# Kernel optimization log

Measured on AMD Instinct MI355X. Metric: run time of the kernel, lower is better.

Reference implementation:

```python
import jax, jax.numpy as jnp
import numpy as np

NUM_DAYOFWEEK, NUM_TIME, NUM_MONTH, NUM_DAY = 7, 24, 12, 31
NUM_DESTINATION = 100000
NUM_FACTOR = 128
NUM_DIM = NUM_FACTOR // 4  # 32
N = 1048576


def setup_inputs() -> dict:
    key = jax.random.key(0)
    ks = jax.random.split(key, 10)
    std = 0.1
    return {
        "dayofweek": jax.random.randint(ks[0], (N,), 0, NUM_DAYOFWEEK),
        "time": jax.random.randint(ks[1], (N,), 0, NUM_TIME),
        "month": jax.random.randint(ks[2], (N,), 0, NUM_MONTH),
        "day": jax.random.randint(ks[3], (N,), 0, NUM_DAY),
        "destination": jax.random.randint(ks[4], (N,), 0, NUM_DESTINATION),
        "W_dayofweek": std * jax.random.normal(ks[5], (NUM_DAYOFWEEK, NUM_DIM), dtype=jnp.float32),
        "W_time": std * jax.random.normal(ks[6], (NUM_TIME, NUM_DIM), dtype=jnp.float32),
        "W_month": std * jax.random.normal(ks[7], (NUM_MONTH, NUM_DIM), dtype=jnp.float32),
        "W_day": std * jax.random.normal(ks[8], (NUM_DAY, NUM_DIM), dtype=jnp.float32),
        "W_item": std * jax.random.normal(ks[9], (NUM_DESTINATION, NUM_FACTOR), dtype=jnp.float32),
    }


def reference(dayofweek, time, month, day, destination,
              W_dayofweek, W_time, W_month, W_day, W_item) -> jnp.ndarray:
    # Gather per-feature embeddings and concat into user vector [N, num_factor]
    user = jnp.concatenate([
        W_dayofweek[dayofweek],  # [N, 32]
        W_time[time],            # [N, 32]
        W_month[month],          # [N, 32]
        W_day[day],              # [N, 32]
    ], axis=-1)
    item = W_item[destination]   # [N, 128]
    # Original: diagonal(mm(user, item.T)) == rowwise dot product; compute it directly.
    return jnp.sum(user * item, axis=-1)  # [N]
```

## Files before the change

kernel.cpp:

```cpp
#include <hip/hip_runtime.h>


typedef unsigned long long u64;
typedef unsigned int uint;
typedef _Float16 half_t;
typedef half_t h2 __attribute__((ext_vector_type(2)));

#if __has_builtin(__builtin_amdgcn_fdot2)
#define HAVE_FDOT2 1
#else
#define HAVE_FDOT2 0
#endif

constexpr int NDIM = 32;
constexpr int SZ_DOW = 7 * NDIM, SZ_TIM = 24 * NDIM, SZ_MON = 12 * NDIM, SZ_DAY = 31 * NDIM;
constexpr int B_DOW = 0;
constexpr int B_TIM = B_DOW + SZ_DOW;
constexpr int B_MON = B_TIM + SZ_TIM;
constexpr int B_DAY = B_MON + SZ_MON;
constexpr int TAB_TOT = B_DAY + SZ_DAY;

constexpr int NB     = 32;
constexpr int DDIV   = 3125;
constexpr int SLICES = 256;
constexpr int SPB    = 4096;
constexpr int BIN_T  = 1024;
constexpr int IPT    = SPB / BIN_T;

__device__ __forceinline__ unsigned short f2h(float f) {
    return __builtin_bit_cast(unsigned short, (half_t)f);
}

__device__ __forceinline__ uint pack2h(float a, float b) {
    return (uint)f2h(a) | ((uint)f2h(b) << 16);
}

__device__ __forceinline__ float dp2(uint a, uint b, float c) {
#if HAVE_FDOT2
    return __builtin_amdgcn_fdot2(__builtin_bit_cast(h2, a), __builtin_bit_cast(h2, b), c, false);
#else
    const h2 x = __builtin_bit_cast(h2, a), y = __builtin_bit_cast(h2, b);
    return c + (float)x.x * (float)y.x + (float)x.y * (float)y.y;
#endif
}

__device__ __forceinline__ float dot16h(uint4 a, uint4 b, uint4 ua, uint4 ub) {
    float s0 = dp2(a.x, ua.x, 0.f);
    float s1 = dp2(a.y, ua.y, 0.f);
    s0 = dp2(a.z, ua.z, s0);
    s1 = dp2(a.w, ua.w, s1);
    s0 = dp2(b.x, ub.x, s0);
    s1 = dp2(b.y, ub.y, s1);
    s0 = dp2(b.z, ub.z, s0);
    s1 = dp2(b.w, ub.w, s1);
    return s0 + s1;
}

__device__ __forceinline__ void load_tab(float* tab, const float* Wdow, const float* Wtim,
                                         const float* Wmon, const float* Wday, int nthr) {
    const int t = threadIdx.x;
    for (int i = t; i < SZ_DOW; i += nthr) tab[B_DOW + i] = Wdow[i];
    for (int i = t; i < SZ_TIM; i += nthr) tab[B_TIM + i] = Wtim[i];
    for (int i = t; i < SZ_MON; i += nthr) tab[B_MON + i] = Wmon[i];
    for (int i = t; i < SZ_DAY; i += nthr) tab[B_DAY + i] = Wday[i];
}

__device__ __forceinline__ void load_tabh(uint* th, const float* W, int base, int sz,
                                          int t, int nthr) {
    const float2* src = (const float2*)W;
    for (int i = t; i < (sz >> 1); i += nthr) {
        const float2 v = src[i];
        th[(base >> 1) + i] = pack2h(v.x, v.y);
    }
}

__global__ __launch_bounds__(BIN_T)
void prep_kernel(const int* __restrict__ dow, const int* __restrict__ tim,
                 const int* __restrict__ mon, const int* __restrict__ day,
                 const int* __restrict__ dest,
                 int2* __restrict__ clG,
                 u64* __restrict__ payload, int n,
                 const float* __restrict__ Witem, unsigned short* __restrict__ Wh,
                 int witem_elems)
{
    __shared__ u64 stage[SPB];
    __shared__ int hist[NB], cursor[NB];

    const int t = threadIdx.x, b = blockIdx.x;
    const int g0 = b * SPB;
    const int rem = n - g0;
    const int len = rem < SPB ? rem : SPB;

    int dreg[IPT], pkreg[IPT];
#pragma unroll
    for (int i = 0; i < IPT; i++) {
        const int k = i * BIN_T + t;
        if (k < len) {
            const int idx = g0 + k;
            dreg[i]  = dest[idx];
            pkreg[i] = dow[idx] | (tim[idx] << 3) | (mon[idx] << 8) | (day[idx] << 12);
        } else { dreg[i] = -1; pkreg[i] = 0; }
    }

    if (Wh) {
        const int nf4   = witem_elems >> 2;
        const int chunk = (nf4 + SLICES - 1) / SLICES;
        const int c0    = b * chunk;
        const int c1    = min(c0 + chunk, nf4);
        const float4* src = (const float4*)Witem;
        ushort4* dst = (ushort4*)Wh;
        for (int i = c0 + t; i < c1; i += BIN_T) {
            const float4 v = src[i];
            ushort4 o;
            o.x = f2h(v.x); o.y = f2h(v.y); o.z = f2h(v.z); o.w = f2h(v.w);
            dst[i] = o;
        }
    }

    if (t < NB) hist[t] = 0;
    __syncthreads();
#pragma unroll
    for (int i = 0; i < IPT; i++)
        if (dreg[i] >= 0) atomicAdd(&hist[dreg[i] / DDIV], 1);
    __syncthreads();
    if (t < 64) {
        int v = (t < NB) ? hist[t] : 0;
#pragma unroll
        for (int d = 1; d < NB; d <<= 1) {
            const int nv = __shfl_up(v, d);
            if (t >= d) v += nv;
        }
        if (t < NB) {
            const int base = v - hist[t];
            cursor[t] = base;
            clG[b * NB + t] = make_int2(hist[t], base);
        }
    }
    __syncthreads();
#pragma unroll
    for (int i = 0; i < IPT; i++) {
        const int k = i * BIN_T + t;
        if (k < len) {
            const int j = atomicAdd(&cursor[dreg[i] / DDIV], 1);
            stage[j] = (u64)(unsigned)(g0 + k)
                     | ((u64)(unsigned)dreg[i]  << 20)
                     | ((u64)(unsigned)pkreg[i] << 37);
        }
    }
    __syncthreads();
#pragma unroll
    for (int i = 0; i < IPT; i++) {
        const int k = i * BIN_T + t;
        if (k < len) payload[g0 + k] = stage[k];
    }
}

__global__ __launch_bounds__(256, 8)
void mf_main_f16(const u64* __restrict__ payload,
                 const float* __restrict__ Wdow, const float* __restrict__ Wtim,
                 const float* __restrict__ Wmon, const float* __restrict__ Wday,
                 const unsigned short* __restrict__ Wh,
                 const int2* __restrict__ clG,
                 float* __restrict__ out)
{
    __shared__ uint tabh[TAB_TOT / 2];

    const int tid = threadIdx.x;
    const int x = blockIdx.x & 7;
    const int s = blockIdx.x >> 3;

    int2 cl[4];
#pragma unroll
    for (int p = 0; p < 4; p++) cl[p] = clG[s * NB + x + 8 * p];

    load_tabh(tabh, Wdow, B_DOW, SZ_DOW, tid, 256);
    load_tabh(tabh, Wtim, B_TIM, SZ_TIM, tid, 256);
    load_tabh(tabh, Wmon, B_MON, SZ_MON, tid, 256);
    load_tabh(tabh, Wday, B_DAY, SZ_DAY, tid, 256);
    __syncthreads();

    const int sub = tid & 63;
    const int wv  = tid >> 6;
    const int g   = sub >> 3;
    const int l8  = sub & 7;
    const int jt   = l8 >> 1;
    const int half = (l8 & 1) * 16;
    const int tbj  = (jt == 0) ? B_DOW : (jt == 1) ? B_TIM : (jt == 2) ? B_MON : B_DAY;
    const int shj  = (jt == 0) ? 37    : (jt == 1) ? 40    : (jt == 2) ? 45    : 49;
    const int mkj  = (jt == 0) ? 7     : (jt == 1) ? 31    : (jt == 2) ? 15    : 31;
    const int tub  = (tbj + half) >> 1;

    for (int p = 0; p < 4; p++) {
        const int L  = cl[p].x;
        const int st = s * SPB + cl[p].y;

        int i = wv * 16;
        u64 p0 = (i + g < L)     ? payload[st + i + g]     : 0ull;
        u64 p1 = (i + 8 + g < L) ? payload[st + i + 8 + g] : 0ull;

        for (; i < L; i += 64) {
            const bool v0 = (i + g) < L, v1 = (i + 8 + g) < L;
            const u64 c0 = p0, c1 = p1;
            const int ni = i + 64;
            p0 = (ni + g < L)     ? payload[st + ni + g]     : 0ull;
            p1 = (ni + 8 + g < L) ? payload[st + ni + 8 + g] : 0ull;

            const int d0 = (int)((c0 >> 20) & 0x1FFFFull);
            const int d1 = (int)((c1 >> 20) & 0x1FFFFull);

            const uint4* r0 = (const uint4*)(Wh + (long)d0 * 128 + (l8 << 4));
            const uint4* r1 = (const uint4*)(Wh + (long)d1 * 128 + (l8 << 4));
            const uint4 A0 = r0[0], B0 = r0[1];
            const uint4 A1 = r1[0], B1 = r1[1];

            const int ix0 = (int)((c0 >> shj) & (u64)mkj);
            const int ix1 = (int)((c1 >> shj) & (u64)mkj);
            const uint4* t0 = (const uint4*)&tabh[tub + ix0 * (NDIM / 2)];
            const uint4* t1 = (const uint4*)&tabh[tub + ix1 * (NDIM / 2)];
            const uint4 U00 = t0[0], U01 = t0[1];
            const uint4 U10 = t1[0], U11 = t1[1];

            float a0 = dot16h(A0, B0, U00, U01);
            float a1 = dot16h(A1, B1, U10, U11);

            a0 += __shfl_xor(a0, 1);  a1 += __shfl_xor(a1, 1);
            a0 += __shfl_xor(a0, 2);  a1 += __shfl_xor(a1, 2);
            a0 += __shfl_xor(a0, 4);  a1 += __shfl_xor(a1, 4);

            if (l8 == 0) {
                if (v0) out[(int)(c0 & 0xFFFFFull)] = a0;
                if (v1) out[(int)(c1 & 0xFFFFFull)] = a1;
            }
        }
    }
}

__global__ __launch_bounds__(256, 8)
void mf_main_f32(const u64* __restrict__ payload,
                 const float* __restrict__ Wdow, const float* __restrict__ Wtim,
                 const float* __restrict__ Wmon, const float* __restrict__ Wday,
                 const float* __restrict__ Witem,
                 const int2* __restrict__ clG,
                 float* __restrict__ out)
{
    __shared__ float tab[TAB_TOT];

    const int tid = threadIdx.x;
    const int x = blockIdx.x & 7;
    const int s = blockIdx.x >> 3;

    int2 cl[4];
#pragma unroll
    for (int p = 0; p < 4; p++) cl[p] = clG[s * NB + x + 8 * p];

    load_tab(tab, Wdow, Wtim, Wmon, Wday, 256);
    __syncthreads();

    const int sub = tid & 63;
    const int wv  = tid >> 6;
    const int g   = sub >> 3;
    const int l8  = sub & 7;
    const int col = l8 * 4;
    const int tb[4] = {B_DOW, B_TIM, B_MON, B_DAY};
    const int sh[4] = {37, 40, 45, 49};
    const int mk[4] = {7, 31, 15, 31};
    for (int p = 0; p < 4; p++) {
        const int L  = cl[p].x;
        const int st = s * SPB + cl[p].y;
        for (int i = wv * 16; i < L; i += 64) {
            const int i0 = i + g, i1 = i + 8 + g;
            const bool v0 = i0 < L, v1 = i1 < L;
            const u64 p0 = v0 ? payload[st + i0] : 0ull;
            const u64 p1 = v1 ? payload[st + i1] : 0ull;
            const int d0 = (int)((p0 >> 20) & 0x1FFFFull);
            const int d1 = (int)((p1 >> 20) & 0x1FFFFull);
            const float* r0 = Witem + (long)d0 * 128 + col;
            const float* r1 = Witem + (long)d1 * 128 + col;
            float4 it0[4], it1[4], us0[4], us1[4];
#pragma unroll
            for (int j = 0; j < 4; j++) it0[j] = *reinterpret_cast<const float4*>(r0 + j * NDIM);
#pragma unroll
            for (int j = 0; j < 4; j++) it1[j] = *reinterpret_cast<const float4*>(r1 + j * NDIM);
#pragma unroll
            for (int j = 0; j < 4; j++) {
                const int idx = (int)((p0 >> sh[j]) & (u64)mk[j]);
                us0[j] = *reinterpret_cast<const float4*>(&tab[tb[j] + idx * NDIM + col]);
            }
#pragma unroll
            for (int j = 0; j < 4; j++) {
                const int idx = (int)((p1 >> sh[j]) & (u64)mk[j]);
                us1[j] = *reinterpret_cast<const float4*>(&tab[tb[j] + idx * NDIM + col]);
            }
            float a0 = 0.f, a1 = 0.f;
#pragma unroll
            for (int j = 0; j < 4; j++) {
                a0 += it0[j].x * us0[j].x + it0[j].y * us0[j].y
                    + it0[j].z * us0[j].z + it0[j].w * us0[j].w;
                a1 += it1[j].x * us1[j].x + it1[j].y * us1[j].y
                    + it1[j].z * us1[j].z + it1[j].w * us1[j].w;
            }
            a0 += __shfl_xor(a0, 1);  a1 += __shfl_xor(a1, 1);
            a0 += __shfl_xor(a0, 2);  a1 += __shfl_xor(a1, 2);
            a0 += __shfl_xor(a0, 4);  a1 += __shfl_xor(a1, 4);
            if (l8 == 0) {
                if (v0) out[(int)(p0 & 0xFFFFFull)] = a0;
                if (v1) out[(int)(p1 & 0xFFFFFull)] = a1;
            }
        }
    }
}

__global__ __launch_bounds__(256, 8)
void mf_dot_kernel(const int* __restrict__ dow, const int* __restrict__ tim,
                   const int* __restrict__ mon, const int* __restrict__ day,
                   const int* __restrict__ dest,
                   const float* __restrict__ Wdow, const float* __restrict__ Wtim,
                   const float* __restrict__ Wmon, const float* __restrict__ Wday,
                   const float* __restrict__ Witem,
                   float* __restrict__ out, int n_samples)
{
    __shared__ float tab[TAB_TOT];
    load_tab(tab, Wdow, Wtim, Wmon, Wday, 256);
    __syncthreads();
    const int tid = threadIdx.x;
    const int lane = tid & 63, sub = lane & 31, wave = tid >> 6, half = lane >> 5;
    const int t = sub >> 3, dofs = (sub & 7) * 4;
    const int* idxp  = (t == 0) ? dow   : (t == 1) ? tim   : (t == 2) ? mon   : day;
    const int  tbase = (t == 0) ? B_DOW : (t == 1) ? B_TIM : (t == 2) ? B_MON : B_DAY;
    long n = (long)blockIdx.x * 8 + wave * 2 + half;
    const long stride = (long)gridDim.x * 8;
    for (; n < n_samples; n += stride) {
        const int idx = idxp[n];
        const int ds  = dest[n];
        const float4 u  = *reinterpret_cast<const float4*>(&tab[tbase + idx * NDIM + dofs]);
        const float4 it = *reinterpret_cast<const float4*>(&Witem[(long)ds * 128 + sub * 4]);
        float r = u.x * it.x + u.y * it.y + u.z * it.z + u.w * it.w;
        r += __shfl_xor(r, 16); r += __shfl_xor(r, 8); r += __shfl_xor(r, 4);
        r += __shfl_xor(r, 2);  r += __shfl_xor(r, 1);
        if (sub == 0) out[n] = r;
    }
}

extern "C" void kernel_launch(void* const* d_in, const int* in_sizes, int n_in,
                              void* d_out, int out_size, void* d_ws, size_t ws_size,
                              hipStream_t stream)
{
    const int*   dow   = (const int*)d_in[0];
    const int*   tim   = (const int*)d_in[1];
    const int*   mon   = (const int*)d_in[2];
    const int*   day   = (const int*)d_in[3];
    const int*   dest  = (const int*)d_in[4];
    const float* Wdow  = (const float*)d_in[5];
    const float* Wtim  = (const float*)d_in[6];
    const float* Wmon  = (const float*)d_in[7];
    const float* Wday  = (const float*)d_in[8];
    const float* Witem = (const float*)d_in[9];
    float* out = (float*)d_out;

    const int n  = in_sizes[0];
    const int we = in_sizes[9];
    const int cap = SLICES * SPB;

    const size_t off_wh       = 64 * 1024;
    const size_t off_pay_full = (off_wh + (size_t)we * 2 + 255) & ~(size_t)255;
    const size_t need_full    = off_pay_full + (size_t)cap * 8;
    const size_t off_pay_mid  = 64 * 1024;
    const size_t need_mid     = off_pay_mid + (size_t)cap * 8;

    if ((size_t)ws_size < need_mid || n > cap) {
        hipLaunchKernelGGL(mf_dot_kernel, dim3(2048), dim3(256), 0, stream,
                           dow, tim, mon, day, dest,
                           Wdow, Wtim, Wmon, Wday, Witem, out, n);
        return;
    }

    const bool full = (size_t)ws_size >= need_full;

    int2* clG = (int2*)d_ws;
    unsigned short* Wh = full ? (unsigned short*)((char*)d_ws + off_wh) : nullptr;
    u64* payload = (u64*)((char*)d_ws + (full ? off_pay_full : off_pay_mid));

    hipLaunchKernelGGL(prep_kernel, dim3(SLICES), dim3(BIN_T), 0, stream,
                       dow, tim, mon, day, dest, clG, payload, n,
                       Witem, Wh, we);
    if (full)
        hipLaunchKernelGGL(mf_main_f16, dim3(SLICES * 8), dim3(256), 0, stream,
                           payload, Wdow, Wtim, Wmon, Wday, Wh, clG, out);
    else
        hipLaunchKernelGGL(mf_main_f32, dim3(SLICES * 8), dim3(256), 0, stream,
                           payload, Wdow, Wtim, Wmon, Wday, Witem, clG, out);
}
```

Baseline: 147.5 us.

## Fuse binning and gather into one kernel, split item-table conversion out

Replaces the prep kernel plus the separate gather kernel with a dedicated f16 conversion kernel and one fused kernel. The fused kernel bins each 2048-sample chunk by destination range in shared memory and gathers straight from that staging buffer, so the global payload array and the cross-block bin metadata are gone. Bins go from 32 to 64 and chunks shrink, with 1024-thread blocks. This removes a global payload write and re-read, but each block now bins over a smaller window, which may give weaker item-row locality, and the conversion becomes a separate launch.

```diff
diff --git a/kernel.cpp b/kernel.cpp
--- a/kernel.cpp
+++ b/kernel.cpp
@@ -20,12 +20,11 @@
 constexpr int B_DAY = B_MON + SZ_MON;
 constexpr int TAB_TOT = B_DAY + SZ_DAY;
 
-constexpr int NB     = 32;
-constexpr int DDIV   = 3125;
-constexpr int SLICES = 256;
-constexpr int SPB    = 4096;
-constexpr int BIN_T  = 1024;
-constexpr int IPT    = SPB / BIN_T;
+constexpr int NB   = 64;
+constexpr int DDIV = 1563;
+constexpr int THR  = 1024;
+constexpr int SPB  = 2048;
+constexpr int IPT  = SPB / THR;
 
 __device__ __forceinline__ unsigned short f2h(float f) {
     return __builtin_bit_cast(unsigned short, (half_t)f);
@@ -74,16 +73,31 @@
     }
 }
 
-__global__ __launch_bounds__(BIN_T)
-void prep_kernel(const int* __restrict__ dow, const int* __restrict__ tim,
-                 const int* __restrict__ mon, const int* __restrict__ day,
-                 const int* __restrict__ dest,
-                 int2* __restrict__ clG,
-                 u64* __restrict__ payload, int n,
-                 const float* __restrict__ Witem, unsigned short* __restrict__ Wh,
-                 int witem_elems)
+__global__ __launch_bounds__(256)
+void convert_kernel(const float* __restrict__ Witem, unsigned short* __restrict__ Wh, int nf4)
+{
+    const float4* src = (const float4*)Witem;
+    ushort4* dst = (ushort4*)Wh;
+    const int stride = gridDim.x * 256;
+    for (int i = blockIdx.x * 256 + threadIdx.x; i < nf4; i += stride) {
+        const float4 v = src[i];
+        ushort4 o;
+        o.x = f2h(v.x); o.y = f2h(v.y); o.z = f2h(v.z); o.w = f2h(v.w);
+        dst[i] = o;
+    }
+}
+
+__global__ __launch_bounds__(THR, 8)
+void bin_gather(const int* __restrict__ dow, const int* __restrict__ tim,
+                const int* __restrict__ mon, const int* __restrict__ day,
+                const int* __restrict__ dest,
+                const float* __restrict__ Wdow, const float* __restrict__ Wtim,
+                const float* __restrict__ Wmon, const float* __restrict__ Wday,
+                const unsigned short* __restrict__ Wh,
+                float* __restrict__ out, int n)
 {
     __shared__ u64 stage[SPB];
+    __shared__ uint tabh[TAB_TOT / 2];
     __shared__ int hist[NB], cursor[NB];
 
     const int t = threadIdx.x, b = blockIdx.x;
@@ -94,7 +108,7 @@
     int dreg[IPT], pkreg[IPT];
 #pragma unroll
     for (int i = 0; i < IPT; i++) {
-        const int k = i * BIN_T + t;
+        const int k = i * THR + t;
         if (k < len) {
             const int idx = g0 + k;
             dreg[i]  = dest[idx];
@@ -102,20 +116,10 @@
         } else { dreg[i] = -1; pkreg[i] = 0; }
     }
 
-    if (Wh) {
-        const int nf4   = witem_elems >> 2;
-        const int chunk = (nf4 + SLICES - 1) / SLICES;
-        const int c0    = b * chunk;
-        const int c1    = min(c0 + chunk, nf4);
-        const float4* src = (const float4*)Witem;
-        ushort4* dst = (ushort4*)Wh;
-        for (int i = c0 + t; i < c1; i += BIN_T) {
-            const float4 v = src[i];
-            ushort4 o;
-            o.x = f2h(v.x); o.y = f2h(v.y); o.z = f2h(v.z); o.w = f2h(v.w);
-            dst[i] = o;
-        }
-    }
+    load_tabh(tabh, Wdow, B_DOW, SZ_DOW, t, THR);
+    load_tabh(tabh, Wtim, B_TIM, SZ_TIM, t, THR);
+    load_tabh(tabh, Wmon, B_MON, SZ_MON, t, THR);
+    load_tabh(tabh, Wday, B_DAY, SZ_DAY, t, THR);
 
     if (t < NB) hist[t] = 0;
     __syncthreads();
@@ -124,22 +128,18 @@
         if (dreg[i] >= 0) atomicAdd(&hist[dreg[i] / DDIV], 1);
     __syncthreads();
     if (t < 64) {
-        int v = (t < NB) ? hist[t] : 0;
-#pragma unroll
-        for (int d = 1; d < NB; d <<= 1) {
+        int v = hist[t];
+#pragma unroll
+        for (int d = 1; d < 64; d <<= 1) {
             const int nv = __shfl_up(v, d);
             if (t >= d) v += nv;
         }
-        if (t < NB) {
-            const int base = v - hist[t];
-            cursor[t] = base;
-            clG[b * NB + t] = make_int2(hist[t], base);
-        }
+        cursor[t] = v - hist[t];
     }
     __syncthreads();
 #pragma unroll
     for (int i = 0; i < IPT; i++) {
-        const int k = i * BIN_T + t;
+        const int k = i * THR + t;
         if (k < len) {
             const int j = atomicAdd(&cursor[dreg[i] / DDIV], 1);
             stage[j] = (u64)(unsigned)(g0 + k)
@@ -148,39 +148,9 @@
         }
     }
     __syncthreads();
-#pragma unroll
-    for (int i = 0; i < IPT; i++) {
-        const int k = i * BIN_T + t;
-        if (k < len) payload[g0 + k] = stage[k];
-    }
-}
-
-__global__ __launch_bounds__(256, 8)
-void mf_main_f16(const u64* __restrict__ payload,
-                 const float* __restrict__ Wdow, const float* __restrict__ Wtim,
-                 const float* __restrict__ Wmon, const float* __restrict__ Wday,
-                 const unsigned short* __restrict__ Wh,
-                 const int2* __restrict__ clG,
-                 float* __restrict__ out)
-{
-    __shared__ uint tabh[TAB_TOT / 2];
-
-    const int tid = threadIdx.x;
-    const int x = blockIdx.x & 7;
-    const int s = blockIdx.x >> 3;
-
-    int2 cl[4];
-#pragma unroll
-    for (int p = 0; p < 4; p++) cl[p] = clG[s * NB + x + 8 * p];
-
-    load_tabh(tabh, Wdow, B_DOW, SZ_DOW, tid, 256);
-    load_tabh(tabh, Wtim, B_TIM, SZ_TIM, tid, 256);
-    load_tabh(tabh, Wmon, B_MON, SZ_MON, tid, 256);
-    load_tabh(tabh, Wday, B_DAY, SZ_DAY, tid, 256);
-    __syncthreads();
-
-    const int sub = tid & 63;
-    const int wv  = tid >> 6;
+
+    const int sub = t & 63;
+    const int wv  = t >> 6;
     const int g   = sub >> 3;
     const int l8  = sub & 7;
     const int jt   = l8 >> 1;
@@ -190,122 +160,37 @@
     const int mkj  = (jt == 0) ? 7     : (jt == 1) ? 31    : (jt == 2) ? 15    : 31;
     const int tub  = (tbj + half) >> 1;
 
-    for (int p = 0; p < 4; p++) {
-        const int L  = cl[p].x;
-        const int st = s * SPB + cl[p].y;
-
-        int i = wv * 16;
-        u64 p0 = (i + g < L)     ? payload[st + i + g]     : 0ull;
-        u64 p1 = (i + 8 + g < L) ? payload[st + i + 8 + g] : 0ull;
-
-        for (; i < L; i += 64) {
-            const bool v0 = (i + g) < L, v1 = (i + 8 + g) < L;
-            const u64 c0 = p0, c1 = p1;
-            const int ni = i + 64;
-            p0 = (ni + g < L)     ? payload[st + ni + g]     : 0ull;
-            p1 = (ni + 8 + g < L) ? payload[st + ni + 8 + g] : 0ull;
-
-            const int d0 = (int)((c0 >> 20) & 0x1FFFFull);
-            const int d1 = (int)((c1 >> 20) & 0x1FFFFull);
-
-            const uint4* r0 = (const uint4*)(Wh + (long)d0 * 128 + (l8 << 4));
-            const uint4* r1 = (const uint4*)(Wh + (long)d1 * 128 + (l8 << 4));
-            const uint4 A0 = r0[0], B0 = r0[1];
-            const uint4 A1 = r1[0], B1 = r1[1];
-
-            const int ix0 = (int)((c0 >> shj) & (u64)mkj);
-            const int ix1 = (int)((c1 >> shj) & (u64)mkj);
-            const uint4* t0 = (const uint4*)&tabh[tub + ix0 * (NDIM / 2)];
-            const uint4* t1 = (const uint4*)&tabh[tub + ix1 * (NDIM / 2)];
-            const uint4 U00 = t0[0], U01 = t0[1];
-            const uint4 U10 = t1[0], U11 = t1[1];
-
-            float a0 = dot16h(A0, B0, U00, U01);
-            float a1 = dot16h(A1, B1, U10, U11);
-
-            a0 += __shfl_xor(a0, 1);  a1 += __shfl_xor(a1, 1);
-            a0 += __shfl_xor(a0, 2);  a1 += __shfl_xor(a1, 2);
-            a0 += __shfl_xor(a0, 4);  a1 += __shfl_xor(a1, 4);
-
-            if (l8 == 0) {
-                if (v0) out[(int)(c0 & 0xFFFFFull)] = a0;
-                if (v1) out[(int)(c1 & 0xFFFFFull)] = a1;
-            }
-        }
-    }
-}
-
-__global__ __launch_bounds__(256, 8)
-void mf_main_f32(const u64* __restrict__ payload,
-                 const float* __restrict__ Wdow, const float* __restrict__ Wtim,
-                 const float* __restrict__ Wmon, const float* __restrict__ Wday,
-                 const float* __restrict__ Witem,
-                 const int2* __restrict__ clG,
-                 float* __restrict__ out)
-{
-    __shared__ float tab[TAB_TOT];
-
-    const int tid = threadIdx.x;
-    const int x = blockIdx.x & 7;
-    const int s = blockIdx.x >> 3;
-
-    int2 cl[4];
-#pragma unroll
-    for (int p = 0; p < 4; p++) cl[p] = clG[s * NB + x + 8 * p];
-
-    load_tab(tab, Wdow, Wtim, Wmon, Wday, 256);
-    __syncthreads();
-
-    const int sub = tid & 63;
-    const int wv  = tid >> 6;
-    const int g   = sub >> 3;
-    const int l8  = sub & 7;
-    const int col = l8 * 4;
-    const int tb[4] = {B_DOW, B_TIM, B_MON, B_DAY};
-    const int sh[4] = {37, 40, 45, 49};
-    const int mk[4] = {7, 31, 15, 31};
-    for (int p = 0; p < 4; p++) {
-        const int L  = cl[p].x;
-        const int st = s * SPB + cl[p].y;
-        for (int i = wv * 16; i < L; i += 64) {
-            const int i0 = i + g, i1 = i + 8 + g;
-            const bool v0 = i0 < L, v1 = i1 < L;
-            const u64 p0 = v0 ? payload[st + i0] : 0ull;
-            const u64 p1 = v1 ? payload[st + i1] : 0ull;
-            const int d0 = (int)((p0 >> 20) & 0x1FFFFull);
-            const int d1 = (int)((p1 >> 20) & 0x1FFFFull);
-            const float* r0 = Witem + (long)d0 * 128 + col;
-            const float* r1 = Witem + (long)d1 * 128 + col;
-            float4 it0[4], it1[4], us0[4], us1[4];
-#pragma unroll
-            for (int j = 0; j < 4; j++) it0[j] = *reinterpret_cast<const float4*>(r0 + j * NDIM);
-#pragma unroll
-            for (int j = 0; j < 4; j++) it1[j] = *reinterpret_cast<const float4*>(r1 + j * NDIM);
-#pragma unroll
-            for (int j = 0; j < 4; j++) {
-                const int idx = (int)((p0 >> sh[j]) & (u64)mk[j]);
-                us0[j] = *reinterpret_cast<const float4*>(&tab[tb[j] + idx * NDIM + col]);
-            }
-#pragma unroll
-            for (int j = 0; j < 4; j++) {
-                const int idx = (int)((p1 >> sh[j]) & (u64)mk[j]);
-                us1[j] = *reinterpret_cast<const float4*>(&tab[tb[j] + idx * NDIM + col]);
-            }
-            float a0 = 0.f, a1 = 0.f;
-#pragma unroll
-            for (int j = 0; j < 4; j++) {
-                a0 += it0[j].x * us0[j].x + it0[j].y * us0[j].y
-                    + it0[j].z * us0[j].z + it0[j].w * us0[j].w;
-                a1 += it1[j].x * us1[j].x + it1[j].y * us1[j].y
-                    + it1[j].z * us1[j].z + it1[j].w * us1[j].w;
-            }
-            a0 += __shfl_xor(a0, 1);  a1 += __shfl_xor(a1, 1);
-            a0 += __shfl_xor(a0, 2);  a1 += __shfl_xor(a1, 2);
-            a0 += __shfl_xor(a0, 4);  a1 += __shfl_xor(a1, 4);
-            if (l8 == 0) {
-                if (v0) out[(int)(p0 & 0xFFFFFull)] = a0;
-                if (v1) out[(int)(p1 & 0xFFFFFull)] = a1;
-            }
+    for (int i = wv * 16; i < len; i += 16 * (THR / 64)) {
+        const int i0 = i + g, i1 = i + 8 + g;
+        const bool v0 = i0 < len, v1 = i1 < len;
+        const u64 c0 = v0 ? stage[i0] : 0ull;
+        const u64 c1 = v1 ? stage[i1] : 0ull;
+
+        const int d0 = (int)((c0 >> 20) & 0x1FFFFull);
+        const int d1 = (int)((c1 >> 20) & 0x1FFFFull);
+
+        const uint4* r0 = (const uint4*)(Wh + (long)d0 * 128 + (l8 << 4));
+        const uint4* r1 = (const uint4*)(Wh + (long)d1 * 128 + (l8 << 4));
+        const uint4 A0 = r0[0], B0 = r0[1];
+        const uint4 A1 = r1[0], B1 = r1[1];
+
+        const int ix0 = (int)((c0 >> shj) & (u64)mkj);
+        const int ix1 = (int)((c1 >> shj) & (u64)mkj);
+        const uint4* t0 = (const uint4*)&tabh[tub + ix0 * (NDIM / 2)];
+        const uint4* t1 = (const uint4*)&tabh[tub + ix1 * (NDIM / 2)];
+        const uint4 U00 = t0[0], U01 = t0[1];
+        const uint4 U10 = t1[0], U11 = t1[1];
+
+        float a0 = dot16h(A0, B0, U00, U01);
+        float a1 = dot16h(A1, B1, U10, U11);
+
+        a0 += __shfl_xor(a0, 1);  a1 += __shfl_xor(a1, 1);
+        a0 += __shfl_xor(a0, 2);  a1 += __shfl_xor(a1, 2);
+        a0 += __shfl_xor(a0, 4);  a1 += __shfl_xor(a1, 4);
+
+        if (l8 == 0) {
+            if (v0) out[(int)(c0 & 0xFFFFFull)] = a0;
+            if (v1) out[(int)(c1 & 0xFFFFFull)] = a1;
         }
     }
 }
@@ -357,36 +242,25 @@
     const float* Witem = (const float*)d_in[9];
     float* out = (float*)d_out;
 
-    const int n  = in_sizes[0];
-    const int we = in_sizes[9];
-    const int cap = SLICES * SPB;
-
-    const size_t off_wh       = 64 * 1024;
-    const size_t off_pay_full = (off_wh + (size_t)we * 2 + 255) & ~(size_t)255;
-    const size_t need_full    = off_pay_full + (size_t)cap * 8;
-    const size_t off_pay_mid  = 64 * 1024;
-    const size_t need_mid     = off_pay_mid + (size_t)cap * 8;
-
-    if ((size_t)ws_size < need_mid || n > cap) {
+    const int n   = in_sizes[0];
+    const int we  = in_sizes[9];
+    const int cap = 1 << 20;
+
+    const size_t need = (size_t)we * 2;
+
+    if ((size_t)ws_size < need || n > cap) {
         hipLaunchKernelGGL(mf_dot_kernel, dim3(2048), dim3(256), 0, stream,
                            dow, tim, mon, day, dest,
                            Wdow, Wtim, Wmon, Wday, Witem, out, n);
         return;
     }
 
-    const bool full = (size_t)ws_size >= need_full;
-
-    int2* clG = (int2*)d_ws;
-    unsigned short* Wh = full ? (unsigned short*)((char*)d_ws + off_wh) : nullptr;
-    u64* payload = (u64*)((char*)d_ws + (full ? off_pay_full : off_pay_mid));
-
-    hipLaunchKernelGGL(prep_kernel, dim3(SLICES), dim3(BIN_T), 0, stream,
-                       dow, tim, mon, day, dest, clG, payload, n,
-                       Witem, Wh, we);
-    if (full)
-        hipLaunchKernelGGL(mf_main_f16, dim3(SLICES * 8), dim3(256), 0, stream,
-                           payload, Wdow, Wtim, Wmon, Wday, Wh, clG, out);
-    else
-        hipLaunchKernelGGL(mf_main_f32, dim3(SLICES * 8), dim3(256), 0, stream,
-                           payload, Wdow, Wtim, Wmon, Wday, Witem, clG, out);
-}
+    unsigned short* Wh = (unsigned short*)d_ws;
+    const int blocks = (n + SPB - 1) / SPB;
+
+    hipLaunchKernelGGL(convert_kernel, dim3(2048), dim3(256), 0, stream,
+                       Witem, Wh, we >> 2);
+    hipLaunchKernelGGL(bin_gather, dim3(blocks), dim3(THR), 0, stream,
+                       dow, tim, mon, day, dest,
+                       Wdow, Wtim, Wmon, Wday, Wh, out, n);
+}
```

After: 150.3 us. No clear change (+2.0%).

## Assign one cluster per wavefront and software-pipeline item row gathers

Applied to the files above, without the earlier changes.

Each wavefront of the f16 main kernel now handles a single cluster instead of all four wavefronts striding through four clusters together. The loop prefetches the next pair of item-row gathers and the payload two steps ahead, so gather latency overlaps the dot-product work. Launch bounds drop from 8 to 6 blocks per SM to leave room for the extra registers these prefetched values need. Work is now balanced per wavefront by cluster size rather than interleaved, which can leave some wavefronts idle if cluster lengths vary.

```diff
diff --git a/kernel.cpp b/kernel.cpp
--- a/kernel.cpp
+++ b/kernel.cpp
@@ -155,7 +155,7 @@
     }
 }
 
-__global__ __launch_bounds__(256, 8)
+__global__ __launch_bounds__(256, 6)
 void mf_main_f16(const u64* __restrict__ payload,
                  const float* __restrict__ Wdow, const float* __restrict__ Wtim,
                  const float* __restrict__ Wmon, const float* __restrict__ Wday,
@@ -168,10 +168,9 @@
     const int tid = threadIdx.x;
     const int x = blockIdx.x & 7;
     const int s = blockIdx.x >> 3;
-
-    int2 cl[4];
-#pragma unroll
-    for (int p = 0; p < 4; p++) cl[p] = clG[s * NB + x + 8 * p];
+    const int wv = tid >> 6;
+
+    const int2 cl = clG[s * NB + x + 8 * wv];
 
     load_tabh(tabh, Wdow, B_DOW, SZ_DOW, tid, 256);
     load_tabh(tabh, Wtim, B_TIM, SZ_TIM, tid, 256);
@@ -180,7 +179,6 @@
     __syncthreads();
 
     const int sub = tid & 63;
-    const int wv  = tid >> 6;
     const int g   = sub >> 3;
     const int l8  = sub & 7;
     const int jt   = l8 >> 1;
@@ -190,28 +188,30 @@
     const int mkj  = (jt == 0) ? 7     : (jt == 1) ? 31    : (jt == 2) ? 15    : 31;
     const int tub  = (tbj + half) >> 1;
 
-    for (int p = 0; p < 4; p++) {
-        const int L  = cl[p].x;
-        const int st = s * SPB + cl[p].y;
-
-        int i = wv * 16;
-        u64 p0 = (i + g < L)     ? payload[st + i + g]     : 0ull;
-        u64 p1 = (i + 8 + g < L) ? payload[st + i + 8 + g] : 0ull;
-
-        for (; i < L; i += 64) {
-            const bool v0 = (i + g) < L, v1 = (i + 8 + g) < L;
-            const u64 c0 = p0, c1 = p1;
-            const int ni = i + 64;
-            p0 = (ni + g < L)     ? payload[st + ni + g]     : 0ull;
-            p1 = (ni + 8 + g < L) ? payload[st + ni + 8 + g] : 0ull;
-
-            const int d0 = (int)((c0 >> 20) & 0x1FFFFull);
-            const int d1 = (int)((c1 >> 20) & 0x1FFFFull);
-
-            const uint4* r0 = (const uint4*)(Wh + (long)d0 * 128 + (l8 << 4));
-            const uint4* r1 = (const uint4*)(Wh + (long)d1 * 128 + (l8 << 4));
-            const uint4 A0 = r0[0], B0 = r0[1];
-            const uint4 A1 = r1[0], B1 = r1[1];
+    const int L  = cl.x;
+    const int st = s * SPB + cl.y;
+
+    u64 c0 = (g < L)      ? payload[st + g]      : 0ull;
+    u64 c1 = (8 + g < L)  ? payload[st + 8 + g]  : 0ull;
+    u64 n0 = (16 + g < L) ? payload[st + 16 + g] : 0ull;
+    u64 n1 = (24 + g < L) ? payload[st + 24 + g] : 0ull;
+    {
+        const int d0 = (int)((c0 >> 20) & 0x1FFFFull);
+        const int d1 = (int)((c1 >> 20) & 0x1FFFFull);
+        const uint4* r0 = (const uint4*)(Wh + (long)d0 * 128 + (l8 << 4));
+        const uint4* r1 = (const uint4*)(Wh + (long)d1 * 128 + (l8 << 4));
+        uint4 A0 = r0[0], B0 = r0[1], A1 = r1[0], B1 = r1[1];
+
+        for (int i = 0; i < L; i += 16) {
+            const int d0n = (int)((n0 >> 20) & 0x1FFFFull);
+            const int d1n = (int)((n1 >> 20) & 0x1FFFFull);
+            const uint4* r0n = (const uint4*)(Wh + (long)d0n * 128 + (l8 << 4));
+            const uint4* r1n = (const uint4*)(Wh + (long)d1n * 128 + (l8 << 4));
+            const uint4 A0n = r0n[0], B0n = r0n[1];
+            const uint4 A1n = r1n[0], B1n = r1n[1];
+            const int pi = i + 32;
+            const u64 m0 = (pi + g < L)     ? payload[st + pi + g]     : 0ull;
+            const u64 m1 = (pi + 8 + g < L) ? payload[st + pi + 8 + g] : 0ull;
 
             const int ix0 = (int)((c0 >> shj) & (u64)mkj);
             const int ix1 = (int)((c1 >> shj) & (u64)mkj);
@@ -228,9 +228,12 @@
             a0 += __shfl_xor(a0, 4);  a1 += __shfl_xor(a1, 4);
 
             if (l8 == 0) {
-                if (v0) out[(int)(c0 & 0xFFFFFull)] = a0;
-                if (v1) out[(int)(c1 & 0xFFFFFull)] = a1;
-            }
+                if (i + g < L)     out[(int)(c0 & 0xFFFFFull)] = a0;
+                if (i + 8 + g < L) out[(int)(c1 & 0xFFFFFull)] = a1;
+            }
+
+            c0 = n0; c1 = n1; n0 = m0; n1 = m1;
+            A0 = A0n; B0 = B0n; A1 = A1n; B1 = B1n;
         }
     }
 }
```

Measured after the change: 147.8 us. No clear change (+0.3%).
